# Performance work log

Hardware: AMD Instinct MI355X
Metric: run time of the kernel (lower is better)

## Reference

```python
import jax, jax.numpy as jnp
import numpy as np

B, T, C = 8, 2048, 768
N_LAYER, LAYER_ID = 12, 0


def setup_inputs() -> dict:
    key = jax.random.key(0)
    ks = jax.random.split(key, 5)
    s = 1.0 / np.sqrt(C)
    x = jax.random.normal(ks[0], (B, T, C), jnp.float32)
    Wk = jax.random.normal(ks[1], (C, C), jnp.float32) * s
    Wv = jax.random.normal(ks[2], (C, C), jnp.float32) * s
    Wr = jax.random.normal(ks[3], (C, C), jnp.float32) * s
    Wo = jax.random.normal(ks[4], (C, C), jnp.float32) * s
    # 'fancy' init for decay / first (layer_id=0 -> ratio_0_to_1 = 0)
    h = np.arange(C, dtype=np.float64)
    decay = (-5.0 + 8.0 * (h / (C - 1)) ** 0.7).astype(np.float32)
    zigzag = (((np.arange(C) + 1) % 3) - 1).astype(np.float64) * 0.5
    first = (np.log(0.3) + zigzag).astype(np.float32)
    return dict(x=x, Wk=Wk, Wv=Wv, Wr=Wr, Wo=Wo,
                decay=jnp.asarray(decay), first=jnp.asarray(first))


def _bi_wkv(w, u, k, v):
    """Bidirectional WKV (Vision-RWKV style), numerically stabilized scans.

    y_t = (sum_{i<t} e^{-(t-1-i)w + k_i} v_i + sum_{i>t} e^{-(i-1-t)w + k_i} v_i
           + e^{u + k_t} v_t) / (same with v_i -> 1).
    k, v: [B,T,C]; w, u: [C].
    """
    kT = jnp.swapaxes(k, 0, 1)  # [T,B,C]
    vT = jnp.swapaxes(v, 0, 1)
    Bb, Cc = kT.shape[1], kT.shape[2]
    NEG = jnp.float32(-1e38)

    def step(carry, inp):
        a, b, p = carry  # a = sum e^{x_i-p} v_i, b = sum e^{x_i-p}, p = running max
        kt, vt = inp
        out = (a, b, p)  # state covers strictly-earlier positions
        p_new = jnp.maximum(p - w, kt)
        e1 = jnp.exp(p - w - p_new)
        e2 = jnp.exp(kt - p_new)
        return (e1 * a + e2 * vt, e1 * b + e2, p_new), out

    init = (jnp.zeros((Bb, Cc), jnp.float32),
            jnp.zeros((Bb, Cc), jnp.float32),
            jnp.full((Bb, Cc), NEG, jnp.float32))
    _, (aL, bL, pL) = jax.lax.scan(step, init, (kT, vT))
    _, (aR, bR, pR) = jax.lax.scan(step, init, (kT[::-1], vT[::-1]))
    aR, bR, pR = aR[::-1], bR[::-1], pR[::-1]

    ps = u + kT  # self term exponent
    q = jnp.maximum(jnp.maximum(pL, pR), ps)
    eL = jnp.exp(pL - q)
    eR = jnp.exp(pR - q)
    eS = jnp.exp(ps - q)
    y = (eL * aL + eR * aR + eS * vT) / (eL * bL + eR * bR + eS)
    return jnp.swapaxes(y, 0, 1)  # [B,T,C]


def reference(x, Wk, Wv, Wr, Wo, decay, first):
    Tlen = x.shape[1]
    # shift_pixel=0 -> xk = xv = xr = x
    k = jnp.einsum('btc,oc->bto', x, Wk)
    v = jnp.einsum('btc,oc->bto', x, Wv)
    sr = jax.nn.sigmoid(jnp.einsum('btc,oc->bto', x, Wr))
    y = _bi_wkv(decay / Tlen, first / Tlen, k, v)
    return jnp.einsum('btj,cj->btc', sr * y, Wo)
```

## Files before the change

### kernel.cpp

```cpp
#include <hip/hip_runtime.h>

#define BSZ 8
#define TLEN 2048
#define CDIM 768
#define LCH 16
#define NCH (TLEN / LCH)

typedef __attribute__((ext_vector_type(4))) float f32x4;
typedef __attribute__((ext_vector_type(8))) _Float16 f16x8;
typedef __attribute__((ext_vector_type(4))) _Float16 f16x4;
typedef __attribute__((ext_vector_type(4))) float float4v;

#define GLD16(g, l)                                                          \
    __builtin_amdgcn_global_load_lds(                                        \
        (const __attribute__((address_space(1))) unsigned int*)(g),          \
        (__attribute__((address_space(3))) unsigned int*)(l), 16, 0, 0)

__global__ __launch_bounds__(256) void split_f16(const float* __restrict__ src,
                                                 _Float16* __restrict__ dst, int n4) {
    int i = blockIdx.x * 256 + threadIdx.x;
    if (i >= n4) return;
    float4v f = ((const float4v*)src)[i];
    f16x4 h;
    #pragma unroll
    for (int j = 0; j < 4; ++j) h[j] = (_Float16)f[j];
    ((f16x4*)dst)[i] = h;
}

__global__ __launch_bounds__(512, 2) void gemm_f16_1p(
    const _Float16* __restrict__ A, const _Float16* __restrict__ W,
    _Float16* __restrict__ o0, _Float16* __restrict__ o1, _Float16* __restrict__ o2,
    float* __restrict__ of32, int mpx, int NTL, int sig_from) {
    constexpr int K = CDIM, N = CDIM;
    constexpr int NT = K / 64;
    __shared__ __align__(16) char smem[147456];

    const int tid  = threadIdx.x;
    const int lane = tid & 63;
    const int wid  = tid >> 6;

    const int bid = blockIdx.x;
    const int xcd = bid & 7;
    const int lj  = bid >> 3;
    const int mt  = lj / NTL;
    const int nt  = lj - mt * NTL;
    const int m0  = (xcd * mpx + mt) * 256;
    const int n0  = nt * 192;

    const bool isA = (wid < 4);
    const int  sw  = wid & 3;
    const char* gsrc = (const char*)(isA ? A : W);
    const int row0 = isA ? (m0 + sw * 64) : (n0 + sw * 48);
    const int gq = (lane & 7) ^ (lane >> 3);
    const size_t gofs = (size_t)(row0 + (lane >> 3)) * (K * 2) + gq * 16;
    const int lofs = (isA ? sw * 8192 : sw * 6144) + lane * 16;

    auto STAGE = [&](int bufbase, int t) {
        char* lb = &smem[bufbase] + lofs;
        const char* g = gsrc + gofs + (size_t)t * 128;
        if (isA) {
            #pragma unroll
            for (int q = 0; q < 8; ++q)
                GLD16(g + q * 12288, lb + q * 1024);
        } else {
            #pragma unroll
            for (int q = 0; q < 6; ++q)
                GLD16(g + q * 12288, lb + q * 1024);
        }
    };

    const int wr = wid >> 1, wc = wid & 1;
    const int rl = lane & 15;
    const int k0ofs = ((((lane >> 4) + 0) ^ (rl & 7)) << 4);
    const int k1ofs = ((((lane >> 4) + 4) ^ (rl & 7)) << 4);

    f32x4 acc[4][6];
    #pragma unroll
    for (int i = 0; i < 4; ++i)
        #pragma unroll
        for (int j = 0; j < 6; ++j)
            acc[i][j] = (f32x4){0.f, 0.f, 0.f, 0.f};

    auto COMPUTE = [&](int ab, int bbase) {
        const char* sb = &smem[0];
        #pragma unroll
        for (int ks = 0; ks < 2; ++ks) {
            const int kq = ks ? k1ofs : k0ofs;
            f16x8 a[4];
            #pragma unroll
            for (int fi = 0; fi < 4; ++fi)
                a[fi] = *(const f16x8*)(sb + ab + (wr * 64 + fi * 16 + rl) * 128 + kq);
            f16x8 bc = *(const f16x8*)(sb + bbase + (wc * 96 + rl) * 128 + kq);
            #pragma unroll
            for (int fj = 0; fj < 6; ++fj) {
                f16x8 bn = bc;
                if (fj < 5)
                    bn = *(const f16x8*)(sb + bbase + (wc * 96 + (fj + 1) * 16 + rl) * 128 + kq);
                __builtin_amdgcn_s_setprio(1);
                #pragma unroll
                for (int fi = 0; fi < 4; ++fi)
                    acc[fi][fj] = __builtin_amdgcn_mfma_f32_16x16x32_f16(a[fi], bc, acc[fi][fj], 0, 0, 0);
                __builtin_amdgcn_s_setprio(0);
                bc = bn;
            }
        }
    };

    if (isA) {
        STAGE(0, 0); STAGE(32768, 1);
        asm volatile("s_waitcnt vmcnt(8)" ::: "memory");
    } else {
        STAGE(98304, 0);
        asm volatile("s_waitcnt vmcnt(0)" ::: "memory");
    }
    __builtin_amdgcn_s_barrier();

    for (int tb = 0; tb < NT; tb += 6) {
        #pragma unroll
        for (int tt = 0; tt < 6; ++tt) {
            const int t = tb + tt;
            if (isA) {
                if (t + 2 < NT) STAGE(((tt + 2) % 3) * 32768, t + 2);
            } else {
                if (t + 1 < NT) STAGE(98304 + ((tt + 1) & 1) * 24576, t + 1);
            }
            COMPUTE((tt % 3) * 32768, 98304 + (tt & 1) * 24576);
            if (isA && t + 2 < NT) asm volatile("s_waitcnt vmcnt(8)" ::: "memory");
            else                   asm volatile("s_waitcnt vmcnt(0)" ::: "memory");
            __builtin_amdgcn_s_barrier();
        }
    }

    const int buf   = nt >> 2;
    const int ncol0 = (nt & 3) * 192;
    const int erow = m0 + wr * 64 + ((lane >> 4) << 2);
    const int ecol = ncol0 + wc * 96 + rl;
    if (of32) {
        #pragma unroll
        for (int fi = 0; fi < 4; ++fi)
            #pragma unroll
            for (int fj = 0; fj < 6; ++fj)
                #pragma unroll
                for (int r = 0; r < 4; ++r)
                    of32[(size_t)(erow + fi * 16 + r) * N + (ecol + fj * 16)] = acc[fi][fj][r];
    } else {
        _Float16* o = (buf == 0) ? o0 : ((buf == 1) ? o1 : o2);
        if (nt >= sig_from) {
            #pragma unroll
            for (int fi = 0; fi < 4; ++fi)
                #pragma unroll
                for (int fj = 0; fj < 6; ++fj)
                    #pragma unroll
                    for (int r = 0; r < 4; ++r)
                        o[(size_t)(erow + fi * 16 + r) * N + (ecol + fj * 16)] =
                            (_Float16)(1.0f / (1.0f + __expf(-acc[fi][fj][r])));
        } else {
            #pragma unroll
            for (int fi = 0; fi < 4; ++fi)
                #pragma unroll
                for (int fj = 0; fj < 6; ++fj)
                    #pragma unroll
                    for (int r = 0; r < 4; ++r)
                        o[(size_t)(erow + fi * 16 + r) * N + (ecol + fj * 16)] =
                            (_Float16)acc[fi][fj][r];
        }
    }
}

#define WKV_STEP(a, bb, p, kt, vt, w)                \
    {                                                \
        const float pn = fmaxf((p) - (w), (kt));     \
        const float e1 = __expf((p) - (w) - pn);     \
        const float e2 = __expf((kt) - pn);          \
        (a)  = e1 * (a)  + e2 * (vt);                \
        (bb) = e1 * (bb) + e2;                       \
        (p)  = pn;                                   \
    }

__global__ __launch_bounds__(256) void wkv_phase1(
    const _Float16* __restrict__ k, const _Float16* __restrict__ v,
    const float* __restrict__ decay,
    float* __restrict__ Sfa, float* __restrict__ Sfb, float* __restrict__ Sfp,
    float* __restrict__ Sba, float* __restrict__ Sbb, float* __restrict__ Sbp) {
    const int c = blockIdx.x * 256 + threadIdx.x;
    const int j = blockIdx.y;
    const int b = blockIdx.z;
    const float w = decay[c] * (1.0f / (float)TLEN);

    const size_t base = ((size_t)b * TLEN + (size_t)j * LCH) * CDIM + c;
    float kt[LCH], vt[LCH];
    #pragma unroll
    for (int i = 0; i < LCH; ++i) {
        kt[i] = (float)k[base + (size_t)i * CDIM];
        vt[i] = (float)v[base + (size_t)i * CDIM];
    }

    const size_t idx = ((size_t)b * NCH + j) * CDIM + c;

    float a = 0.0f, bb = 0.0f, p = -1e38f;
    #pragma unroll
    for (int i = 0; i < LCH; ++i) WKV_STEP(a, bb, p, kt[i], vt[i], w);
    Sfa[idx] = a; Sfb[idx] = bb; Sfp[idx] = p;

    a = 0.0f; bb = 0.0f; p = -1e38f;
    #pragma unroll
    for (int i = LCH - 1; i >= 0; --i) WKV_STEP(a, bb, p, kt[i], vt[i], w);
    Sba[idx] = a; Sbb[idx] = bb; Sbp[idx] = p;
}

#define WKV_COMBINE(a, bb, p, as, bs, ps, wL)        \
    {                                                \
        const float pn = fmaxf((p) - (wL), (ps));    \
        const float e1 = __expf((p) - (wL) - pn);    \
        const float e2 = __expf((ps) - pn);          \
        (a)  = e1 * (a)  + e2 * (as);                \
        (bb) = e1 * (bb) + e2 * (bs);                \
        (p)  = pn;                                   \
    }

__global__ __launch_bounds__(64) void wkv_phase2(
    const float* __restrict__ Sfa, const float* __restrict__ Sfb, const float* __restrict__ Sfp,
    const float* __restrict__ Sba, const float* __restrict__ Sbb, const float* __restrict__ Sbp,
    const float* __restrict__ decay,
    float* __restrict__ Lina, float* __restrict__ Linb, float* __restrict__ Linp,
    float* __restrict__ Rina, float* __restrict__ Rinb, float* __restrict__ Rinp) {
    const int c = blockIdx.x * 64 + threadIdx.x;
    const int b = blockIdx.y;
    const int dir = blockIdx.z;
    const float wL = decay[c] * ((float)LCH / (float)TLEN);

    const float* Sa = dir ? Sba : Sfa;
    const float* Sb = dir ? Sbb : Sfb;
    const float* Sp = dir ? Sbp : Sfp;
    float* Oa = dir ? Rina : Lina;
    float* Ob = dir ? Rinb : Linb;
    float* Op = dir ? Rinp : Linp;

    const size_t base = (size_t)b * NCH * CDIM + c;
    auto IDX = [&](int j) {
        return base + (size_t)(dir ? (NCH - 1 - j) : j) * CDIM;
    };

    float gaA[4], gbA[4], gpA[4], gaB[4], gbB[4], gpB[4];
    #pragma unroll
    for (int u = 0; u < 4; ++u) {
        const size_t id = IDX(u);
        gaA[u] = Sa[id]; gbA[u] = Sb[id]; gpA[u] = Sp[id];
    }
    float a = 0.0f, bb = 0.0f, p = -1e38f;

    for (int jg = 0; jg < NCH; jg += 8) {
        #pragma unroll
        for (int u = 0; u < 4; ++u) {
            const size_t id = IDX(jg + 4 + u);
            gaB[u] = Sa[id]; gbB[u] = Sb[id]; gpB[u] = Sp[id];
        }
        #pragma unroll
        for (int u = 0; u < 4; ++u) {
            const size_t id = IDX(jg + u);
            Oa[id] = a; Ob[id] = bb; Op[id] = p;
            WKV_COMBINE(a, bb, p, gaA[u], gbA[u], gpA[u], wL);
        }
        if (jg + 8 < NCH) {
            #pragma unroll
            for (int u = 0; u < 4; ++u) {
                const size_t id = IDX(jg + 8 + u);
                gaA[u] = Sa[id]; gbA[u] = Sb[id]; gpA[u] = Sp[id];
            }
        }
        #pragma unroll
        for (int u = 0; u < 4; ++u) {
            const size_t id = IDX(jg + 4 + u);
            Oa[id] = a; Ob[id] = bb; Op[id] = p;
            WKV_COMBINE(a, bb, p, gaB[u], gbB[u], gpB[u], wL);
        }
    }
}

__global__ __launch_bounds__(256) void wkv_phase3(
    const _Float16* __restrict__ k, const _Float16* __restrict__ v,
    const _Float16* __restrict__ sr,
    const float* __restrict__ Lina, const float* __restrict__ Linb, const float* __restrict__ Linp,
    const float* __restrict__ Rina, const float* __restrict__ Rinb, const float* __restrict__ Rinp,
    const float* __restrict__ decay, const float* __restrict__ first,
    _Float16* __restrict__ zh) {
    const int c = blockIdx.x * 256 + threadIdx.x;
    const int j = blockIdx.y;
    const int b = blockIdx.z;
    const float w = decay[c] * (1.0f / (float)TLEN);
    const float u = first[c] * (1.0f / (float)TLEN);

    const size_t base = ((size_t)b * TLEN + (size_t)j * LCH) * CDIM + c;
    float kt[LCH], vt[LCH];
    #pragma unroll
    for (int i = 0; i < LCH; ++i) {
        kt[i] = (float)k[base + (size_t)i * CDIM];
        vt[i] = (float)v[base + (size_t)i * CDIM];
    }

    const size_t idx = ((size_t)b * NCH + j) * CDIM + c;

    float ar[LCH], br[LCH], pr[LCH];
    {
        float a = Rina[idx], bb = Rinb[idx], p = Rinp[idx];
        #pragma unroll
        for (int i = LCH - 1; i >= 0; --i) {
            ar[i] = a; br[i] = bb; pr[i] = p;
            WKV_STEP(a, bb, p, kt[i], vt[i], w);
        }
    }
    {
        float a = Lina[idx], bb = Linb[idx], p = Linp[idx];
        #pragma unroll
        for (int i = 0; i < LCH; ++i) {
            const size_t off = base + (size_t)i * CDIM;
            const float srt = (float)sr[off];
            const float ps = u + kt[i];
            const float q  = fmaxf(fmaxf(p, pr[i]), ps);
            const float eL = __expf(p - q);
            const float eR = __expf(pr[i] - q);
            const float eS = __expf(ps - q);
            const float num = eL * a  + eR * ar[i] + eS * vt[i];
            const float den = eL * bb + eR * br[i] + eS;
            zh[off] = (_Float16)(srt * (num / den));
            WKV_STEP(a, bb, p, kt[i], vt[i], w);
        }
    }
}

extern "C" void kernel_launch(void* const* d_in, const int* in_sizes, int n_in,
                              void* d_out, int out_size, void* d_ws, size_t ws_size,
                              hipStream_t stream) {
    const float* x     = (const float*)d_in[0];
    const float* Wk    = (const float*)d_in[1];
    const float* Wv    = (const float*)d_in[2];
    const float* Wr    = (const float*)d_in[3];
    const float* Wo    = (const float*)d_in[4];
    const float* decay = (const float*)d_in[5];
    const float* first = (const float*)d_in[6];
    float* out = (float*)d_out;

    const size_t WN = (size_t)CDIM * CDIM;
    const size_t wbytes = 4 * WN * sizeof(_Float16);
    const size_t per_b  = (size_t)TLEN * CDIM * 8 + 12ull * NCH * CDIM * 4;
    if (ws_size < wbytes + per_b) return;
    int nb = (int)((ws_size - wbytes) / per_b);
    if (nb > BSZ) nb = BSZ;

    _Float16* wsp  = (_Float16*)d_ws;
    _Float16* Wcat = wsp;
    _Float16* Woh  = wsp + 3 * WN;

    const size_t NE = (size_t)nb * TLEN * CDIM;
    const size_t NP = (size_t)nb * NCH * CDIM;
    float* Sfa = (float*)(wsp + 4 * WN);
    float* Sfb = Sfa + NP;  float* Sfp = Sfb + NP;
    float* Sba = Sfp + NP;  float* Sbb = Sba + NP;  float* Sbp = Sbb + NP;
    float* Lina = Sbp + NP; float* Linb = Lina + NP; float* Linp = Linb + NP;
    float* Rina = Linp + NP; float* Rinb = Rina + NP; float* Rinp = Rinb + NP;
    _Float16* kh  = (_Float16*)(Rinp + NP);
    _Float16* vh  = kh + NE;
    _Float16* srh = vh + NE;
    _Float16* xh  = srh + NE;
    _Float16* zh  = xh;

    split_f16<<<dim3((int)(WN / 1024)), dim3(256), 0, stream>>>(Wk, Wcat + 0 * WN, (int)(WN / 4));
    split_f16<<<dim3((int)(WN / 1024)), dim3(256), 0, stream>>>(Wv, Wcat + 1 * WN, (int)(WN / 4));
    split_f16<<<dim3((int)(WN / 1024)), dim3(256), 0, stream>>>(Wr, Wcat + 2 * WN, (int)(WN / 4));
    split_f16<<<dim3((int)(WN / 1024)), dim3(256), 0, stream>>>(Wo, Woh, (int)(WN / 4));

    for (int b0 = 0; b0 < BSZ; b0 += nb) {
        const int curb = (BSZ - b0 < nb) ? (BSZ - b0) : nb;
        const int rows = curb * TLEN;
        const float* xc = x   + (size_t)b0 * TLEN * CDIM;
        float*       oc = out + (size_t)b0 * TLEN * CDIM;

        const int n4 = rows * CDIM / 4;
        split_f16<<<dim3(n4 / 256), dim3(256), 0, stream>>>(xc, xh, n4);

        const int mtiles = rows / 256;
        const int mpx    = mtiles / 8;

        gemm_f16_1p<<<dim3(mtiles * 12), dim3(512), 0, stream>>>(
            xh, Wcat, kh, vh, srh, nullptr, mpx, 12, 8);

        wkv_phase1<<<dim3(CDIM / 256, NCH, curb), dim3(256), 0, stream>>>(
            kh, vh, decay, Sfa, Sfb, Sfp, Sba, Sbb, Sbp);
        wkv_phase2<<<dim3(CDIM / 64, curb, 2), dim3(64), 0, stream>>>(
            Sfa, Sfb, Sfp, Sba, Sbb, Sbp, decay,
            Lina, Linb, Linp, Rina, Rinb, Rinp);
        wkv_phase3<<<dim3(CDIM / 256, NCH, curb), dim3(256), 0, stream>>>(
            kh, vh, srh, Lina, Linb, Linp, Rina, Rinb, Rinp, decay, first, zh);

        gemm_f16_1p<<<dim3(mtiles * 4), dim3(512), 0, stream>>>(
            zh, Woh, nullptr, nullptr, nullptr, oc, mpx, 4, 99);
    }
}
```

Before: 173.6 us.

## Rewrite GEMM as 256x256 tile with 4-phase interleaved prefetch pipeline

```diff
diff --git a/kernel.cpp b/kernel.cpp
--- a/kernel.cpp
+++ b/kernel.cpp
@@ -27,142 +27,137 @@
     ((f16x4*)dst)[i] = h;
 }
 
-__global__ __launch_bounds__(512, 2) void gemm_f16_1p(
+__global__ __launch_bounds__(512, 2) void gemm_8ph(
     const _Float16* __restrict__ A, const _Float16* __restrict__ W,
     _Float16* __restrict__ o0, _Float16* __restrict__ o1, _Float16* __restrict__ o2,
-    float* __restrict__ of32, int mpx, int NTL, int sig_from) {
-    constexpr int K = CDIM, N = CDIM;
+    float* __restrict__ of32, int mpx, int NTL) {
+    constexpr int K = CDIM;
     constexpr int NT = K / 64;
-    __shared__ __align__(16) char smem[147456];
+    __shared__ __align__(16) char smem[131072];
 
     const int tid  = threadIdx.x;
     const int lane = tid & 63;
     const int wid  = tid >> 6;
-
-    const int bid = blockIdx.x;
-    const int xcd = bid & 7;
-    const int lj  = bid >> 3;
-    const int mt  = lj / NTL;
-    const int nt  = lj - mt * NTL;
-    const int m0  = (xcd * mpx + mt) * 256;
-    const int n0  = nt * 192;
-
-    const bool isA = (wid < 4);
-    const int  sw  = wid & 3;
-    const char* gsrc = (const char*)(isA ? A : W);
-    const int row0 = isA ? (m0 + sw * 64) : (n0 + sw * 48);
-    const int gq = (lane & 7) ^ (lane >> 3);
-    const size_t gofs = (size_t)(row0 + (lane >> 3)) * (K * 2) + gq * 16;
-    const int lofs = (isA ? sw * 8192 : sw * 6144) + lane * 16;
-
-    auto STAGE = [&](int bufbase, int t) {
-        char* lb = &smem[bufbase] + lofs;
-        const char* g = gsrc + gofs + (size_t)t * 128;
-        if (isA) {
-            #pragma unroll
-            for (int q = 0; q < 8; ++q)
-                GLD16(g + q * 12288, lb + q * 1024);
-        } else {
-            #pragma unroll
-            for (int q = 0; q < 6; ++q)
-                GLD16(g + q * 12288, lb + q * 1024);
-        }
+    const int bid  = blockIdx.x;
+    const int xcd  = bid & 7;
+    const int lj   = bid >> 3;
+    const int mt   = lj / NTL;
+    const int nt   = lj - mt * NTL;
+    const int m0   = (xcd * mpx + mt) * 256;
+    const int n0   = nt * 256;
+
+    const int r0 = tid >> 3;
+    const int c0 = (tid & 7) ^ (r0 & 7);
+    const int s1 = tid + 512;
+    const int r1 = s1 >> 3;
+    const int c1 = (s1 & 7) ^ (r1 & 7);
+    const char* gA = (const char*)A;
+    const char* gW = (const char*)W;
+
+    auto STAGE_HALF = [&](int bufb, int q, int t) {
+        const bool isA = (q < 2);
+        const char* g = isA ? gA : gW;
+        const int rowb = (isA ? m0 : n0) + (q & 1) * 128;
+        char* l = &smem[bufb + q * 16384];
+        GLD16(g + (size_t)((rowb + r0) * (K * 2) + c0 * 16 + t * 128), l + tid * 16);
+        GLD16(g + (size_t)((rowb + r1) * (K * 2) + c1 * 16 + t * 128), l + s1 * 16);
     };
 
-    const int wr = wid >> 1, wc = wid & 1;
+    const int wr = wid >> 2;
+    const int wc = wid & 3;
     const int rl = lane & 15;
-    const int k0ofs = ((((lane >> 4) + 0) ^ (rl & 7)) << 4);
-    const int k1ofs = ((((lane >> 4) + 4) ^ (rl & 7)) << 4);
-
-    f32x4 acc[4][6];
-    #pragma unroll
-    for (int i = 0; i < 4; ++i)
-        #pragma unroll
-        for (int j = 0; j < 6; ++j)
+    const int kc0 = (((lane >> 4)    ) ^ (rl & 7)) << 4;
+    const int kc1 = (((lane >> 4) + 4) ^ (rl & 7)) << 4;
+
+    f32x4 acc[8][4];
+    #pragma unroll
+    for (int i = 0; i < 8; ++i)
+        #pragma unroll
+        for (int j = 0; j < 4; ++j)
             acc[i][j] = (f32x4){0.f, 0.f, 0.f, 0.f};
 
-    auto COMPUTE = [&](int ab, int bbase) {
-        const char* sb = &smem[0];
-        #pragma unroll
-        for (int ks = 0; ks < 2; ++ks) {
-            const int kq = ks ? k1ofs : k0ofs;
-            f16x8 a[4];
-            #pragma unroll
-            for (int fi = 0; fi < 4; ++fi)
-                a[fi] = *(const f16x8*)(sb + ab + (wr * 64 + fi * 16 + rl) * 128 + kq);
-            f16x8 bc = *(const f16x8*)(sb + bbase + (wc * 96 + rl) * 128 + kq);
-            #pragma unroll
-            for (int fj = 0; fj < 6; ++fj) {
-                f16x8 bn = bc;
-                if (fj < 5)
-                    bn = *(const f16x8*)(sb + bbase + (wc * 96 + (fj + 1) * 16 + rl) * 128 + kq);
-                __builtin_amdgcn_s_setprio(1);
-                #pragma unroll
-                for (int fi = 0; fi < 4; ++fi)
-                    acc[fi][fj] = __builtin_amdgcn_mfma_f32_16x16x32_f16(a[fi], bc, acc[fi][fj], 0, 0, 0);
-                __builtin_amdgcn_s_setprio(0);
-                bc = bn;
+    #pragma unroll
+    for (int q = 0; q < 4; ++q) STAGE_HALF(0, q, 0);
+    asm volatile("s_waitcnt vmcnt(0)" ::: "memory");
+    __builtin_amdgcn_s_barrier();
+
+    for (int t = 0; t < NT; ++t) {
+        const int db  = (t & 1) << 16;
+        const int nb2 = db ^ 65536;
+        const char* sb = &smem[db];
+        f16x8 breg[4][2];
+
+        #pragma unroll
+        for (int q = 0; q < 4; ++q) {
+            f16x8 areg[2][2];
+            #pragma unroll
+            for (int mi = 0; mi < 2; ++mi) {
+                const int ro = (wr * 128 + (2 * q + mi) * 16 + rl) * 128;
+                areg[mi][0] = *(const f16x8*)(sb + ro + kc0);
+                areg[mi][1] = *(const f16x8*)(sb + ro + kc1);
             }
-        }
-    };
-
-    if (isA) {
-        STAGE(0, 0); STAGE(32768, 1);
-        asm volatile("s_waitcnt vmcnt(8)" ::: "memory");
+            if (q == 0) {
+                #pragma unroll
+                for (int nf = 0; nf < 4; ++nf) {
+                    const int ro = 32768 + (wc * 64 + nf * 16 + rl) * 128;
+                    breg[nf][0] = *(const f16x8*)(sb + ro + kc0);
+                    breg[nf][1] = *(const f16x8*)(sb + ro + kc1);
+                }
+            }
+            if (t + 1 < NT) STAGE_HALF(nb2, q, t + 1);
+
+            __builtin_amdgcn_s_barrier();
+            asm volatile("s_waitcnt lgkmcnt(0)" ::: "memory");
+            __builtin_amdgcn_sched_barrier(0);
+            __builtin_amdgcn_s_setprio(1);
+            #pragma unroll
+            for (int mi = 0; mi < 2; ++mi)
+                #pragma unroll
+                for (int nf = 0; nf < 4; ++nf) {
+                    acc[2 * q + mi][nf] = __builtin_amdgcn_mfma_f32_16x16x32_f16(
+                        areg[mi][0], breg[nf][0], acc[2 * q + mi][nf], 0, 0, 0);
+                    acc[2 * q + mi][nf] = __builtin_amdgcn_mfma_f32_16x16x32_f16(
+                        areg[mi][1], breg[nf][1], acc[2 * q + mi][nf], 0, 0, 0);
+                }
+            __builtin_amdgcn_s_setprio(0);
+            if (q == 3) asm volatile("s_waitcnt vmcnt(0)" ::: "memory");
+            __builtin_amdgcn_s_barrier();
+        }
+    }
+
+    const int erow0 = m0 + wr * 128 + ((lane >> 4) << 2);
+    if (of32) {
+        const int col0 = n0 + wc * 64 + rl;
+        #pragma unroll
+        for (int mf = 0; mf < 8; ++mf)
+            #pragma unroll
+            for (int nf = 0; nf < 4; ++nf)
+                #pragma unroll
+                for (int r = 0; r < 4; ++r)
+                    of32[(size_t)(erow0 + mf * 16 + r) * CDIM + (col0 + nf * 16)] =
+                        acc[mf][nf][r];
     } else {
-        STAGE(98304, 0);
-        asm volatile("s_waitcnt vmcnt(0)" ::: "memory");
-    }
-    __builtin_amdgcn_s_barrier();
-
-    for (int tb = 0; tb < NT; tb += 6) {
-        #pragma unroll
-        for (int tt = 0; tt < 6; ++tt) {
-            const int t = tb + tt;
-            if (isA) {
-                if (t + 2 < NT) STAGE(((tt + 2) % 3) * 32768, t + 2);
-            } else {
-                if (t + 1 < NT) STAGE(98304 + ((tt + 1) & 1) * 24576, t + 1);
-            }
-            COMPUTE((tt % 3) * 32768, 98304 + (tt & 1) * 24576);
-            if (isA && t + 2 < NT) asm volatile("s_waitcnt vmcnt(8)" ::: "memory");
-            else                   asm volatile("s_waitcnt vmcnt(0)" ::: "memory");
-            __builtin_amdgcn_s_barrier();
-        }
-    }
-
-    const int buf   = nt >> 2;
-    const int ncol0 = (nt & 3) * 192;
-    const int erow = m0 + wr * 64 + ((lane >> 4) << 2);
-    const int ecol = ncol0 + wc * 96 + rl;
-    if (of32) {
-        #pragma unroll
-        for (int fi = 0; fi < 4; ++fi)
-            #pragma unroll
-            for (int fj = 0; fj < 6; ++fj)
-                #pragma unroll
-                for (int r = 0; r < 4; ++r)
-                    of32[(size_t)(erow + fi * 16 + r) * N + (ecol + fj * 16)] = acc[fi][fj][r];
-    } else {
-        _Float16* o = (buf == 0) ? o0 : ((buf == 1) ? o1 : o2);
-        if (nt >= sig_from) {
-            #pragma unroll
-            for (int fi = 0; fi < 4; ++fi)
-                #pragma unroll
-                for (int fj = 0; fj < 6; ++fj)
+        const int mat  = nt / 3;
+        const int col0 = (nt - mat * 3) * 256 + wc * 64 + rl;
+        _Float16* o = (mat == 0) ? o0 : ((mat == 1) ? o1 : o2);
+        if (mat == 2) {
+            #pragma unroll
+            for (int mf = 0; mf < 8; ++mf)
+                #pragma unroll
+                for (int nf = 0; nf < 4; ++nf)
                     #pragma unroll
                     for (int r = 0; r < 4; ++r)
-                        o[(size_t)(erow + fi * 16 + r) * N + (ecol + fj * 16)] =
-                            (_Float16)(1.0f / (1.0f + __expf(-acc[fi][fj][r])));
+                        o[(size_t)(erow0 + mf * 16 + r) * CDIM + (col0 + nf * 16)] =
+                            (_Float16)(1.0f / (1.0f + __expf(-acc[mf][nf][r])));
         } else {
             #pragma unroll
-            for (int fi = 0; fi < 4; ++fi)
-                #pragma unroll
-                for (int fj = 0; fj < 6; ++fj)
+            for (int mf = 0; mf < 8; ++mf)
+                #pragma unroll
+                for (int nf = 0; nf < 4; ++nf)
                     #pragma unroll
                     for (int r = 0; r < 4; ++r)
-                        o[(size_t)(erow + fi * 16 + r) * N + (ecol + fj * 16)] =
-                            (_Float16)acc[fi][fj][r];
+                        o[(size_t)(erow0 + mf * 16 + r) * CDIM + (col0 + nf * 16)] =
+                            (_Float16)acc[mf][nf][r];
         }
     }
 }
@@ -381,8 +376,8 @@
         const int mtiles = rows / 256;
         const int mpx    = mtiles / 8;
 
-        gemm_f16_1p<<<dim3(mtiles * 12), dim3(512), 0, stream>>>(
-            xh, Wcat, kh, vh, srh, nullptr, mpx, 12, 8);
+        gemm_8ph<<<dim3(mtiles * 9), dim3(512), 0, stream>>>(
+            xh, Wcat, kh, vh, srh, nullptr, mpx, 9);
 
         wkv_phase1<<<dim3(CDIM / 256, NCH, curb), dim3(256), 0, stream>>>(
             kh, vh, decay, Sfa, Sfb, Sfp, Sba, Sbb, Sbp);
@@ -392,7 +387,7 @@
         wkv_phase3<<<dim3(CDIM / 256, NCH, curb), dim3(256), 0, stream>>>(
             kh, vh, srh, Lina, Linb, Linp, Rina, Rinb, Rinp, decay, first, zh);
 
-        gemm_f16_1p<<<dim3(mtiles * 4), dim3(512), 0, stream>>>(
-            zh, Woh, nullptr, nullptr, nullptr, oc, mpx, 4, 99);
-    }
-}
+        gemm_8ph<<<dim3(mtiles * 3), dim3(512), 0, stream>>>(
+            zh, Woh, nullptr, nullptr, nullptr, oc, mpx, 3);
+    }
+}
```

New measurement: 190.2 us. 1.1x slower.
